# Performance work log

Hardware: AMD Instinct MI355X
Metric: run time of the kernel (lower is better)

The kernel has to match this reference:

```python
import jax, jax.numpy as jnp
import numpy as np

N_NODES = 100000
N_EDGES = 1600000
IN_F, HID_F, OUT_F = 64, 64, 64


def setup_inputs() -> dict:
    key = jax.random.key(0)
    ks = jax.random.split(key, 9)
    return {
        "x": jax.random.normal(ks[0], (N_NODES, IN_F), dtype=jnp.float32),
        "src": jax.random.randint(ks[1], (N_EDGES,), 0, N_NODES, dtype=jnp.int64),
        "dst": jax.random.randint(ks[2], (N_EDGES,), 0, N_NODES, dtype=jnp.int64),
        "W_self1": jax.random.normal(ks[3], (IN_F, HID_F), dtype=jnp.float32) * (1.0 / np.sqrt(IN_F)),
        "W_neigh1": jax.random.normal(ks[4], (IN_F, HID_F), dtype=jnp.float32) * (1.0 / np.sqrt(IN_F)),
        "b1": jnp.zeros((HID_F,), dtype=jnp.float32),
        "W_self2": jax.random.normal(ks[5], (HID_F, OUT_F), dtype=jnp.float32) * (1.0 / np.sqrt(HID_F)),
        "W_neigh2": jax.random.normal(ks[6], (HID_F, OUT_F), dtype=jnp.float32) * (1.0 / np.sqrt(HID_F)),
        "b2": jnp.zeros((OUT_F,), dtype=jnp.float32),
    }


def reference(x, src, dst, W_self1, W_neigh1, b1, W_self2, W_neigh2, b2):
    N = x.shape[0]
    # in-degree per destination node; zero-in-degree nodes get zero aggregate (DGL semantics)
    deg = jax.ops.segment_sum(jnp.ones(dst.shape, dtype=x.dtype), dst, num_segments=N)
    inv_deg = jnp.where(deg > 0, 1.0 / jnp.maximum(deg, 1.0), 0.0)[:, None]  # [N,1]

    def sage_conv(h, W_s, W_n, b):
        # mean over in-neighbors: gather src feats, segment-sum at dst, normalize
        agg = jax.ops.segment_sum(h[src], dst, num_segments=N) * inv_deg  # [N,F]
        return h @ W_s + agg @ W_n + b

    h = jax.nn.relu(sage_conv(x, W_self1, W_neigh1, b1))
    return sage_conv(h, W_self2, W_neigh2, b2)
```

## Files before the change

kernel.cpp:

```cpp
#include <hip/hip_runtime.h>

#define N_NODES 100000
#define N_EDGES 1600000
#define NBKT 196
#define BKT_SHIFT 9
#define BKT_MASK 511
#define DL_SHIFT 17
#define SRC_MASK 0x1FFFF
#define NT_TILES 6250
#define CNT_BLOCKS 256
#define CVT_BLOCKS 1563

typedef __attribute__((ext_vector_type(8))) short short8;
typedef __attribute__((ext_vector_type(4))) float float4v;

__device__ __forceinline__ unsigned short f2bf(float f) {
  unsigned u = __float_as_uint(f);
  return (unsigned short)((u + 0x7fffu + ((u >> 16) & 1u)) >> 16);
}
__device__ __forceinline__ float bflo(unsigned d) { return __uint_as_float(d << 16); }
__device__ __forceinline__ float bfhi(unsigned d) { return __uint_as_float(d & 0xffff0000u); }

__device__ __forceinline__ void acc_add(float a[8], uint4 v) {
  a[0] += bflo(v.x); a[1] += bfhi(v.x);
  a[2] += bflo(v.y); a[3] += bfhi(v.y);
  a[4] += bflo(v.z); a[5] += bfhi(v.z);
  a[6] += bflo(v.w); a[7] += bfhi(v.w);
}
__device__ __forceinline__ void acc_fma(float a[8], uint4 v, float m) {
  a[0] = fmaf(m, bflo(v.x), a[0]); a[1] = fmaf(m, bfhi(v.x), a[1]);
  a[2] = fmaf(m, bflo(v.y), a[2]); a[3] = fmaf(m, bfhi(v.y), a[3]);
  a[4] = fmaf(m, bflo(v.z), a[4]); a[5] = fmaf(m, bfhi(v.z), a[5]);
  a[6] = fmaf(m, bflo(v.w), a[6]); a[7] = fmaf(m, bfhi(v.w), a[7]);
}


__global__ void k_prep_count(const float* __restrict__ in, unsigned short* __restrict__ outb,
                             const float* __restrict__ W0, const float* __restrict__ W1,
                             const float* __restrict__ W2, const float* __restrict__ W3,
                             unsigned short* __restrict__ F,
                             const int* __restrict__ dst, int* __restrict__ blkCnt) {
  __shared__ int hist[NBKT];
  const int bid = blockIdx.x;
  if (bid < CNT_BLOCKS) {
    for (int t = threadIdx.x; t < NBKT; t += 256) hist[t] = 0;
    __syncthreads();
    const int e0 = bid * (N_EDGES / CNT_BLOCKS);
    const int e1 = e0 + (N_EDGES / CNT_BLOCKS);
    for (int e = e0 + threadIdx.x; e < e1; e += 256)
      atomicAdd(&hist[dst[e] >> BKT_SHIFT], 1);
    __syncthreads();
    for (int t = threadIdx.x; t < NBKT; t += 256)
      blkCnt[t * CNT_BLOCKS + bid] = hist[t];
    return;
  }
  if (bid < CNT_BLOCKS + 4) {
    if (threadIdx.x >= 64) return;
    const int wsel = bid - CNT_BLOCKS;
    const float* W = (wsel == 0) ? W0 : (wsel == 1) ? W1 : (wsel == 2) ? W2 : W3;
    unsigned short* out = F + wsel * 4096;
    int lane = threadIdx.x;
    int col = lane & 15, kr = lane >> 4;
    #pragma unroll
    for (int kc = 0; kc < 2; kc++)
      #pragma unroll
      for (int nt = 0; nt < 4; nt++) {
        unsigned d[4];
        #pragma unroll
        for (int jj = 0; jj < 4; jj++) {
          float w0 = W[(kc * 32 + kr * 8 + 2 * jj)     * 64 + nt * 16 + col];
          float w1 = W[(kc * 32 + kr * 8 + 2 * jj + 1) * 64 + nt * 16 + col];
          d[jj] = ((unsigned)f2bf(w1) << 16) | f2bf(w0);
        }
        uint4* p = (uint4*)(out + ((kc * 4 + nt) * 64 + lane) * 8);
        *p = make_uint4(d[0], d[1], d[2], d[3]);
      }
    return;
  }
  const int base = (bid - CNT_BLOCKS - 4) * 1024 + threadIdx.x;
  #pragma unroll
  for (int j = 0; j < 4; j++) {
    int i = base + j * 256;
    if (i < 1600000) {
      float4 v = ((const float4*)in)[i];
      unsigned d0 = ((unsigned)f2bf(v.y) << 16) | f2bf(v.x);
      unsigned d1 = ((unsigned)f2bf(v.w) << 16) | f2bf(v.z);
      ((uint2*)outb)[i] = make_uint2(d0, d1);
    }
  }
}


__global__ void kA_scan1(int* __restrict__ blkCnt, int* __restrict__ bktTot) {
  const int b = blockIdx.x;
  const int tid = threadIdx.x, lane = tid & 63, w = tid >> 6;
  int v = blkCnt[b * CNT_BLOCKS + tid];
  int inc = v;
  #pragma unroll
  for (int d = 1; d < 64; d <<= 1) { int y = __shfl_up(inc, d); if (lane >= d) inc += y; }
  __shared__ int wtot[4];
  if (lane == 63) wtot[w] = inc;
  __syncthreads();
  int base = 0;
  for (int j = 0; j < w; j++) base += wtot[j];
  blkCnt[b * CNT_BLOCKS + tid] = base + inc - v;
  if (tid == CNT_BLOCKS - 1) bktTot[b] = base + inc;
}


__global__ void kA_scatter(const int* __restrict__ src, const int* __restrict__ dst,
                           const int* __restrict__ blkCnt, const int* __restrict__ bktTot,
                           int* __restrict__ bktStart, int* __restrict__ binned) {
  __shared__ int ps[NBKT];
  __shared__ int curb[NBKT];
  const int tid = threadIdx.x;
  if (tid < 64) {
    int running = 0;
    for (int base = 0; base < NBKT; base += 64) {
      int i = base + tid;
      int v = (i < NBKT) ? bktTot[i] : 0;
      int inc = v;
      #pragma unroll
      for (int d = 1; d < 64; d <<= 1) { int y = __shfl_up(inc, d); if (tid >= d) inc += y; }
      if (i < NBKT) ps[i] = running + inc - v;
      running += __shfl(inc, 63);
    }
  }
  __syncthreads();
  for (int t = tid; t < NBKT; t += 256)
    curb[t] = ps[t] + blkCnt[t * CNT_BLOCKS + blockIdx.x];
  if (blockIdx.x == 0)
    for (int t = tid; t < NBKT; t += 256) bktStart[t] = ps[t];
  __syncthreads();
  const int e0 = blockIdx.x * (N_EDGES / CNT_BLOCKS);
  const int e1 = e0 + (N_EDGES / CNT_BLOCKS);
  for (int e = e0 + tid; e < e1; e += 256) {
    int d = dst[e];
    int s = src[e];
    int b = d >> BKT_SHIFT;
    int p = atomicAdd(&curb[b], 1);
    binned[p] = s | ((d & BKT_MASK) << DL_SHIFT);
  }
}


__global__ __launch_bounds__(512)
void k_sort(const int* __restrict__ binned, const int* __restrict__ bktStart,
            const int* __restrict__ bktTot,
            int* __restrict__ off, int* __restrict__ esrc) {
  const int b = blockIdx.x;
  const int tid = threadIdx.x, lane = tid & 63, w = tid >> 6;
  __shared__ int cnt[512];
  __shared__ int pos[512];
  __shared__ int wtot[8];
  cnt[tid] = 0;
  __syncthreads();
  const int s0 = bktStart[b], ne = bktTot[b];
  for (int i = tid; i < ne; i += 512)
    atomicAdd(&cnt[binned[s0 + i] >> DL_SHIFT], 1);
  __syncthreads();
  int c = cnt[tid];
  int inc = c;
  #pragma unroll
  for (int d = 1; d < 64; d <<= 1) { int y = __shfl_up(inc, d); if (lane >= d) inc += y; }
  if (lane == 63) wtot[w] = inc;
  __syncthreads();
  int base = s0;
  for (int j = 0; j < w; j++) base += wtot[j];
  int ex = base + inc - c;
  pos[tid] = ex;
  int n0 = (b << BKT_SHIFT) + tid;
  if (n0 < N_NODES) off[n0] = ex;
  if (b == NBKT - 1 && tid == 0) off[N_NODES] = N_EDGES;
  if (b == NBKT - 1 && tid < 4) esrc[N_EDGES + tid] = 0;
  __syncthreads();
  for (int i = tid; i < ne; i += 512) {
    int pe = binned[s0 + i];
    int p = atomicAdd(&pos[pe >> DL_SHIFT], 1);
    esrc[p] = pe & SRC_MASK;
  }
}


template <bool RELU, bool OUT_BF>
__global__ void k_fused(const unsigned short* __restrict__ featb,
                        const int* __restrict__ off, const int* __restrict__ esrc,
                        const unsigned short* __restrict__ wfS,
                        const unsigned short* __restrict__ wfN,
                        const float* __restrict__ bias,
                        float* __restrict__ outf, unsigned short* __restrict__ outb) {
  __shared__ unsigned short aggl[4][16 * 64];
  const int tid = threadIdx.x;
  const int lane = tid & 63;
  const int wslot = tid >> 6;
  const int t = (blockIdx.x * blockDim.x + tid) >> 6;
  if (t >= NT_TILES) return;

  unsigned short* lw = &aggl[wslot][0];
  const int n = lane >> 3;
  const int h = lane & 7;

  #pragma unroll
  for (int half = 0; half < 2; ++half) {
    const int row = half * 8 + n;
    const int node = t * 16 + row;
    const int o0 = off[node];
    const int o1 = off[node + 1];
    float a[8];
    #pragma unroll
    for (int q = 0; q < 8; q++) a[q] = 0.f;

    int i = o0;
    int s0e = esrc[i], s1e = esrc[i + 1], s2e = esrc[i + 2], s3e = esrc[i + 3];
    for (; i + 4 <= o1; ) {
      uint4 v0 = *(const uint4*)(featb + s0e * 64 + h * 8);
      uint4 v1 = *(const uint4*)(featb + s1e * 64 + h * 8);
      uint4 v2 = *(const uint4*)(featb + s2e * 64 + h * 8);
      uint4 v3 = *(const uint4*)(featb + s3e * 64 + h * 8);
      i += 4;
      s0e = esrc[i]; s1e = esrc[i + 1]; s2e = esrc[i + 2]; s3e = esrc[i + 3];
      acc_add(a, v0); acc_add(a, v1); acc_add(a, v2); acc_add(a, v3);
    }
    if (i < o1) {
      const int rem = o1 - i;
      int t1 = (rem > 1) ? s1e : s0e;
      int t2 = (rem > 2) ? s2e : s0e;
      float m1 = (rem > 1) ? 1.f : 0.f;
      float m2 = (rem > 2) ? 1.f : 0.f;
      uint4 v0 = *(const uint4*)(featb + s0e * 64 + h * 8);
      uint4 v1 = *(const uint4*)(featb + t1 * 64 + h * 8);
      uint4 v2 = *(const uint4*)(featb + t2 * 64 + h * 8);
      acc_add(a, v0); acc_fma(a, v1, m1); acc_fma(a, v2, m2);
    }

    const int dg = o1 - o0;
    const float inv = (dg > 0) ? (1.0f / (float)dg) : 0.f;
    unsigned d0 = ((unsigned)f2bf(a[1] * inv) << 16) | f2bf(a[0] * inv);
    unsigned d1 = ((unsigned)f2bf(a[3] * inv) << 16) | f2bf(a[2] * inv);
    unsigned d2 = ((unsigned)f2bf(a[5] * inv) << 16) | f2bf(a[4] * inv);
    unsigned d3 = ((unsigned)f2bf(a[7] * inv) << 16) | f2bf(a[6] * inv);
    *(uint4*)(lw + row * 64 + ((h ^ (row & 7)) << 3)) = make_uint4(d0, d1, d2, d3);
  }

  __builtin_amdgcn_wave_barrier();
  asm volatile("" ::: "memory");

  const int col = lane & 15, rr = lane >> 4;
  const int m = t * 16 + col;
  short8 as0 = *(const short8*)(featb + m * 64 + rr * 8);
  short8 as1 = *(const short8*)(featb + m * 64 + 32 + rr * 8);
  short8 aa0 = *(const short8*)(lw + col * 64 + ((rr ^ (col & 7)) << 3));
  short8 aa1 = *(const short8*)(lw + col * 64 + (((rr + 4) ^ (col & 7)) << 3));

  #pragma unroll
  for (int nt = 0; nt < 4; nt++) {
    short8 bs0 = *(const short8*)(wfS + ((0 * 4 + nt) * 64 + lane) * 8);
    short8 bs1 = *(const short8*)(wfS + ((1 * 4 + nt) * 64 + lane) * 8);
    short8 bn0 = *(const short8*)(wfN + ((0 * 4 + nt) * 64 + lane) * 8);
    short8 bn1 = *(const short8*)(wfN + ((1 * 4 + nt) * 64 + lane) * 8);
    float bvn = bias[nt * 16 + col];
    float4v cfr = {bvn, bvn, bvn, bvn};
    cfr = __builtin_amdgcn_mfma_f32_16x16x32_bf16(as0, bs0, cfr, 0, 0, 0);
    cfr = __builtin_amdgcn_mfma_f32_16x16x32_bf16(as1, bs1, cfr, 0, 0, 0);
    cfr = __builtin_amdgcn_mfma_f32_16x16x32_bf16(aa0, bn0, cfr, 0, 0, 0);
    cfr = __builtin_amdgcn_mfma_f32_16x16x32_bf16(aa1, bn1, cfr, 0, 0, 0);
    #pragma unroll
    for (int r2 = 0; r2 < 4; r2++) {
      int row = t * 16 + rr * 4 + r2;
      float v = cfr[r2];
      if (RELU) v = fmaxf(v, 0.f);
      if (OUT_BF) outb[row * 64 + nt * 16 + col] = f2bf(v);
      else        outf[row * 64 + nt * 16 + col] = v;
    }
  }
}


extern "C" void kernel_launch(void* const* d_in, const int* in_sizes, int n_in,
                              void* d_out, int out_size, void* d_ws, size_t ws_size,
                              hipStream_t stream) {
  const float* x   = (const float*)d_in[0];
  const int*   src = (const int*)d_in[1];
  const int*   dst = (const int*)d_in[2];
  const float* Ws1 = (const float*)d_in[3];
  const float* Wn1 = (const float*)d_in[4];
  const float* b1  = (const float*)d_in[5];
  const float* Ws2 = (const float*)d_in[6];
  const float* Wn2 = (const float*)d_in[7];
  const float* b2  = (const float*)d_in[8];

  char* ws = (char*)d_ws;
  int*            blkCnt   = (int*)(ws + 0);
  int*            bktTot   = (int*)(ws + 200704);
  int*            bktStart = (int*)(ws + 201488);
  unsigned short* wf       = (unsigned short*)(ws + 202272);
  int*            off      = (int*)(ws + 235040);
  int*            binned   = (int*)(ws + 635072);
  int*            esrc     = (int*)(ws + 7035072);
  unsigned short* xbf      = (unsigned short*)(ws + 13435136);
  unsigned short* hbf      = (unsigned short*)(ws + 26235136);

  k_prep_count<<<CNT_BLOCKS + 4 + CVT_BLOCKS, 256, 0, stream>>>(
      x, xbf, Ws1, Wn1, Ws2, Wn2, wf, dst, blkCnt);
  kA_scan1<<<NBKT, CNT_BLOCKS, 0, stream>>>(blkCnt, bktTot);
  kA_scatter<<<CNT_BLOCKS, 256, 0, stream>>>(src, dst, blkCnt, bktTot, bktStart, binned);
  k_sort<<<NBKT, 512, 0, stream>>>(binned, bktStart, bktTot, off, esrc);

  k_fused<true, true><<<1563, 256, 0, stream>>>(xbf, off, esrc, wf + 0 * 4096,
                                                wf + 1 * 4096, b1, nullptr, hbf);
  k_fused<false, false><<<1563, 256, 0, stream>>>(hbf, off, esrc, wf + 2 * 4096,
                                                  wf + 3 * 4096, b2, (float*)d_out, nullptr);
}
```

Before: 200.1 us.

## Pad per-node edge lists to multiples of four with dummy zero node

```diff
diff --git a/kernel.cpp b/kernel.cpp
--- a/kernel.cpp
+++ b/kernel.cpp
@@ -10,6 +10,7 @@
 #define NT_TILES 6250
 #define CNT_BLOCKS 256
 #define CVT_BLOCKS 1563
+#define ST_MASK 0x1FFFFF
 
 typedef __attribute__((ext_vector_type(8))) short short8;
 typedef __attribute__((ext_vector_type(4))) float float4v;
@@ -27,15 +28,10 @@
   a[4] += bflo(v.z); a[5] += bfhi(v.z);
   a[6] += bflo(v.w); a[7] += bfhi(v.w);
 }
-__device__ __forceinline__ void acc_fma(float a[8], uint4 v, float m) {
-  a[0] = fmaf(m, bflo(v.x), a[0]); a[1] = fmaf(m, bfhi(v.x), a[1]);
-  a[2] = fmaf(m, bflo(v.y), a[2]); a[3] = fmaf(m, bfhi(v.y), a[3]);
-  a[4] = fmaf(m, bflo(v.z), a[4]); a[5] = fmaf(m, bfhi(v.z), a[5]);
-  a[6] = fmaf(m, bflo(v.w), a[6]); a[7] = fmaf(m, bfhi(v.w), a[7]);
-}
 
 
 __global__ void k_prep_count(const float* __restrict__ in, unsigned short* __restrict__ outb,
+                             unsigned short* __restrict__ hbfz,
                              const float* __restrict__ W0, const float* __restrict__ W1,
                              const float* __restrict__ W2, const float* __restrict__ W3,
                              unsigned short* __restrict__ F,
@@ -55,8 +51,15 @@
     return;
   }
   if (bid < CNT_BLOCKS + 4) {
-    if (threadIdx.x >= 64) return;
     const int wsel = bid - CNT_BLOCKS;
+    if (threadIdx.x >= 64) {
+      if (wsel == 0 && threadIdx.x < 96) {
+        int j = threadIdx.x - 64;
+        ((unsigned*)(outb + (size_t)N_NODES * 64))[j] = 0;
+        ((unsigned*)(hbfz + (size_t)N_NODES * 64))[j] = 0;
+      }
+      return;
+    }
     const float* W = (wsel == 0) ? W0 : (wsel == 1) ? W1 : (wsel == 2) ? W2 : W3;
     unsigned short* out = F + wsel * 4096;
     int lane = threadIdx.x;
@@ -147,7 +150,7 @@
 __global__ __launch_bounds__(512)
 void k_sort(const int* __restrict__ binned, const int* __restrict__ bktStart,
             const int* __restrict__ bktTot,
-            int* __restrict__ off, int* __restrict__ esrc) {
+            unsigned* __restrict__ offp, int* __restrict__ esrc) {
   const int b = blockIdx.x;
   const int tid = threadIdx.x, lane = tid & 63, w = tid >> 6;
   __shared__ int cnt[512];
@@ -159,20 +162,20 @@
   for (int i = tid; i < ne; i += 512)
     atomicAdd(&cnt[binned[s0 + i] >> DL_SHIFT], 1);
   __syncthreads();
-  int c = cnt[tid];
-  int inc = c;
+  const int c = cnt[tid];
+  const int c4 = (c + 3) & ~3;
+  int inc = c4;
   #pragma unroll
   for (int d = 1; d < 64; d <<= 1) { int y = __shfl_up(inc, d); if (lane >= d) inc += y; }
   if (lane == 63) wtot[w] = inc;
   __syncthreads();
-  int base = s0;
+  int base = ((s0 + 3) & ~3) + 1536 * b;
   for (int j = 0; j < w; j++) base += wtot[j];
-  int ex = base + inc - c;
-  pos[tid] = ex;
-  int n0 = (b << BKT_SHIFT) + tid;
-  if (n0 < N_NODES) off[n0] = ex;
-  if (b == NBKT - 1 && tid == 0) off[N_NODES] = N_EDGES;
-  if (b == NBKT - 1 && tid < 4) esrc[N_EDGES + tid] = 0;
+  const int st = base + inc - c4;
+  pos[tid] = st;
+  const int n0 = (b << BKT_SHIFT) + tid;
+  if (n0 < N_NODES) offp[n0] = (unsigned)st | ((unsigned)c << 21);
+  for (int k = c; k < c4; k++) esrc[st + k] = N_NODES;
   __syncthreads();
   for (int i = tid; i < ne; i += 512) {
     int pe = binned[s0 + i];
@@ -184,7 +187,7 @@
 
 template <bool RELU, bool OUT_BF>
 __global__ void k_fused(const unsigned short* __restrict__ featb,
-                        const int* __restrict__ off, const int* __restrict__ esrc,
+                        const unsigned* __restrict__ offp, const int* __restrict__ esrc,
                         const unsigned short* __restrict__ wfS,
                         const unsigned short* __restrict__ wfN,
                         const float* __restrict__ bias,
@@ -204,36 +207,26 @@
   for (int half = 0; half < 2; ++half) {
     const int row = half * 8 + n;
     const int node = t * 16 + row;
-    const int o0 = off[node];
-    const int o1 = off[node + 1];
+    const unsigned wrd = offp[node];
+    const int o0 = (int)(wrd & ST_MASK);
+    const int dg = (int)(wrd >> 21);
+    const int o1p = o0 + ((dg + 3) & ~3);
     float a[8];
     #pragma unroll
-    for (int q = 0; q < 8; q++) a[q] = 0.f;
+    for (int q8 = 0; q8 < 8; q8++) a[q8] = 0.f;
 
     int i = o0;
-    int s0e = esrc[i], s1e = esrc[i + 1], s2e = esrc[i + 2], s3e = esrc[i + 3];
-    for (; i + 4 <= o1; ) {
-      uint4 v0 = *(const uint4*)(featb + s0e * 64 + h * 8);
-      uint4 v1 = *(const uint4*)(featb + s1e * 64 + h * 8);
-      uint4 v2 = *(const uint4*)(featb + s2e * 64 + h * 8);
-      uint4 v3 = *(const uint4*)(featb + s3e * 64 + h * 8);
+    int4 q = *(const int4*)(esrc + i);
+    for (; i < o1p; ) {
+      uint4 v0 = *(const uint4*)(featb + q.x * 64 + h * 8);
+      uint4 v1 = *(const uint4*)(featb + q.y * 64 + h * 8);
+      uint4 v2 = *(const uint4*)(featb + q.z * 64 + h * 8);
+      uint4 v3 = *(const uint4*)(featb + q.w * 64 + h * 8);
       i += 4;
-      s0e = esrc[i]; s1e = esrc[i + 1]; s2e = esrc[i + 2]; s3e = esrc[i + 3];
+      q = *(const int4*)(esrc + i);
       acc_add(a, v0); acc_add(a, v1); acc_add(a, v2); acc_add(a, v3);
     }
-    if (i < o1) {
-      const int rem = o1 - i;
-      int t1 = (rem > 1) ? s1e : s0e;
-      int t2 = (rem > 2) ? s2e : s0e;
-      float m1 = (rem > 1) ? 1.f : 0.f;
-      float m2 = (rem > 2) ? 1.f : 0.f;
-      uint4 v0 = *(const uint4*)(featb + s0e * 64 + h * 8);
-      uint4 v1 = *(const uint4*)(featb + t1 * 64 + h * 8);
-      uint4 v2 = *(const uint4*)(featb + t2 * 64 + h * 8);
-      acc_add(a, v0); acc_fma(a, v1, m1); acc_fma(a, v2, m2);
-    }
-
-    const int dg = o1 - o0;
+
     const float inv = (dg > 0) ? (1.0f / (float)dg) : 0.f;
     unsigned d0 = ((unsigned)f2bf(a[1] * inv) << 16) | f2bf(a[0] * inv);
     unsigned d1 = ((unsigned)f2bf(a[3] * inv) << 16) | f2bf(a[2] * inv);
@@ -294,20 +287,20 @@
   int*            bktTot   = (int*)(ws + 200704);
   int*            bktStart = (int*)(ws + 201488);
   unsigned short* wf       = (unsigned short*)(ws + 202272);
-  int*            off      = (int*)(ws + 235040);
+  unsigned*       offp     = (unsigned*)(ws + 235040);
   int*            binned   = (int*)(ws + 635072);
   int*            esrc     = (int*)(ws + 7035072);
-  unsigned short* xbf      = (unsigned short*)(ws + 13435136);
-  unsigned short* hbf      = (unsigned short*)(ws + 26235136);
+  unsigned short* xbf      = (unsigned short*)(ws + 14643392);
+  unsigned short* hbf      = (unsigned short*)(ws + 27443584);
 
   k_prep_count<<<CNT_BLOCKS + 4 + CVT_BLOCKS, 256, 0, stream>>>(
-      x, xbf, Ws1, Wn1, Ws2, Wn2, wf, dst, blkCnt);
+      x, xbf, hbf, Ws1, Wn1, Ws2, Wn2, wf, dst, blkCnt);
   kA_scan1<<<NBKT, CNT_BLOCKS, 0, stream>>>(blkCnt, bktTot);
   kA_scatter<<<CNT_BLOCKS, 256, 0, stream>>>(src, dst, blkCnt, bktTot, bktStart, binned);
-  k_sort<<<NBKT, 512, 0, stream>>>(binned, bktStart, bktTot, off, esrc);
-
-  k_fused<true, true><<<1563, 256, 0, stream>>>(xbf, off, esrc, wf + 0 * 4096,
+  k_sort<<<NBKT, 512, 0, stream>>>(binned, bktStart, bktTot, offp, esrc);
+
+  k_fused<true, true><<<1563, 256, 0, stream>>>(xbf, offp, esrc, wf + 0 * 4096,
                                                 wf + 1 * 4096, b1, nullptr, hbf);
-  k_fused<false, false><<<1563, 256, 0, stream>>>(hbf, off, esrc, wf + 2 * 4096,
+  k_fused<false, false><<<1563, 256, 0, stream>>>(hbf, offp, esrc, wf + 2 * 4096,
                                                   wf + 3 * 4096, b2, (float*)d_out, nullptr);
 }
```

Result: slower. 216.9 us (+8.4%).
